# Performance work log

Measured on AMD Instinct MI355X. Metric: run time of the kernel, lower is better.

## Reference

```python
import jax, jax.numpy as jnp
import numpy as np

D = 1024      # n_embd
H = 2048      # expert_hidden_dim
G = 4         # num_groups
EPG = 2       # experts_per_group
NH = 16       # num_heads
HD = D // NH  # head dim
L = 4         # num_layers
V = 32000     # vocab_size
NC = 32000    # num_classes
MAXS = 2048   # max_seq_len
B, S = 2, 1024
TEMP = 1.0    # router_temperature


def setup_inputs() -> dict:
    key = jax.random.key(0)
    ks = jax.random.split(key, 12)
    sc = 0.02
    def n(k, shape):
        return jax.random.normal(k, shape, jnp.float32) * sc
    return {
        "x": jax.random.randint(ks[0], (B, S), 0, V),
        "tok_emb": n(ks[1], (V, D)),
        "pos_emb": n(ks[2], (MAXS, D)),
        "in_proj_w": n(ks[3], (L, 3 * D, D)),
        "in_proj_b": jnp.zeros((L, 3 * D)),
        "out_w": n(ks[4], (L, D, D)),
        "out_b": jnp.zeros((L, D)),
        "ln1_w": jnp.ones((L, D)), "ln1_b": jnp.zeros((L, D)),
        "ln2_w": jnp.ones((L, D)), "ln2_b": jnp.zeros((L, D)),
        "gr_w": n(ks[5], (L, D, G)), "gr_b": jnp.zeros((L, G)),
        "er_w": n(ks[6], (L, G, D, EPG)), "er_b": jnp.zeros((L, G, EPG)),
        "w1": n(ks[7], (L, G, EPG, D, H)), "b1": jnp.zeros((L, G, EPG, H)),
        "w2": n(ks[8], (L, G, EPG, H, D)), "b2": jnp.zeros((L, G, EPG, D)),
        "lnf_w": jnp.ones((D,)), "lnf_b": jnp.zeros((D,)),
        "head_w": n(ks[9], (NC, D)), "head_b": jnp.zeros((NC,)),
    }


def _ln(x, w, b):
    m = x.mean(-1, keepdims=True)
    v = ((x - m) ** 2).mean(-1, keepdims=True)
    return (x - m) * jax.lax.rsqrt(v + 1e-5) * w + b


def _attn(x, wqkv, bqkv, wo, bo, mask):
    b, s, _ = x.shape
    qkv = x @ wqkv.T + bqkv
    q, k, v = jnp.split(qkv, 3, axis=-1)
    def heads(t):
        return t.reshape(b, s, NH, HD).transpose(0, 2, 1, 3)
    q, k, v = heads(q), heads(k), heads(v)
    sc = jnp.einsum('bhqd,bhkd->bhqk', q, k) / np.float32(np.sqrt(HD))
    sc = jnp.where(mask, sc, jnp.float32(-1e30))
    a = jax.nn.softmax(sc, axis=-1)
    o = jnp.einsum('bhqk,bhkd->bhqd', a, v).transpose(0, 2, 1, 3).reshape(b, s, D)
    return o @ wo.T + bo


def _moe(x, gw, gb, ew, eb, w1, b1, w2, b2):
    # x: [T, D] flattened tokens. 2-level routing: top-1 group, top-1 expert in group.
    gp = jax.nn.softmax((x @ gw + gb) / TEMP, axis=-1)                      # [T,G]
    gidx = jnp.argmax(gp, axis=-1)                                          # [T]
    ep = jax.nn.softmax((jnp.einsum('td,gde->tge', x, ew) + eb) / TEMP, -1)  # [T,G,EPG]
    ep_sel = jnp.take_along_axis(ep, gidx[:, None, None], axis=1)[:, 0]     # [T,EPG]
    eidx = jnp.argmax(ep_sel, axis=-1)                                      # [T]
    gate = (jnp.take_along_axis(gp, gidx[:, None], 1)[:, 0]
            * jnp.take_along_axis(ep_sel, eidx[:, None], 1)[:, 0])          # [T]
    hmid = jax.nn.relu(jnp.einsum('td,gedh->tgeh', x, w1) + b1)             # [T,G,EPG,H]
    out = jnp.einsum('tgeh,gehd->tged', hmid, w2) + b2                      # [T,G,EPG,D]
    comb = (jax.nn.one_hot(gidx, G, dtype=x.dtype)[:, :, None]
            * jax.nn.one_hot(eidx, EPG, dtype=x.dtype)[:, None, :]) * gate[:, None, None]
    return jnp.einsum('tge,tged->td', comb, out)


def reference(x, tok_emb, pos_emb, in_proj_w, in_proj_b, out_w, out_b,
              ln1_w, ln1_b, ln2_w, ln2_b, gr_w, gr_b, er_w, er_b,
              w1, b1, w2, b2, lnf_w, lnf_b, head_w, head_b):
    b, s = x.shape
    h = tok_emb[x] + pos_emb[jnp.arange(s)][None]
    mask = jnp.tril(jnp.ones((s, s), bool))
    for l in range(L):
        x1 = _ln(h, ln1_w[l], ln1_b[l])
        h = h + _attn(x1, in_proj_w[l], in_proj_b[l], out_w[l], out_b[l], mask)
        x2 = _ln(h, ln2_w[l], ln2_b[l]).reshape(b * s, D)
        h = h + _moe(x2, gr_w[l], gr_b[l], er_w[l], er_b[l],
                     w1[l], b1[l], w2[l], b2[l]).reshape(b, s, D)
    h = _ln(h, lnf_w, lnf_b).mean(axis=1)
    return h @ head_w.T + head_b
```

## Files before the change

kernel.cpp:

```cpp
#include <hip/hip_runtime.h>
#include <hip/hip_bf16.h>
#include <cstdint>
#include <cstddef>

#define D_   1024
#define H_   2048
#define G_   4
#define EPG_ 2
#define NE_  8
#define NH_  16
#define HD_  64
#define L_   4
#define V_   32000
#define NC_  32000
#define B_   2
#define S_   1024
#define T_   2048
#define MAXBLK_ 24

typedef __attribute__((__ext_vector_type__(8))) __bf16 bf16x8;
typedef __attribute__((__ext_vector_type__(4))) __bf16 bf16x4;
typedef __attribute__((__ext_vector_type__(4))) float  f32x4;

__device__ __forceinline__ void gl_lds16(const void* g, void* l) {
  __builtin_amdgcn_global_load_lds(
      (const __attribute__((address_space(1))) void*)g,
      (__attribute__((address_space(3))) void*)l, 16, 0, 0);
}

__device__ __forceinline__ float wave_sum(float v) {
  #pragma unroll
  for (int o = 32; o >= 1; o >>= 1) v += __shfl_xor(v, o, 64);
  return v;
}

__global__ __launch_bounds__(256) void embed_kernel(const int* __restrict__ x,
    const float* __restrict__ tok, const float* __restrict__ pos,
    float* __restrict__ h) {
  int t = blockIdx.x;
  int tid = threadIdx.x;
  int token = x[t];
  int s = t & (S_ - 1);
  float4 tv = *(const float4*)(tok + (size_t)token * D_ + tid * 4);
  float4 pv = *(const float4*)(pos + (size_t)s * D_ + tid * 4);
  float4 r;
  r.x = tv.x + pv.x; r.y = tv.y + pv.y; r.z = tv.z + pv.z; r.w = tv.w + pv.w;
  *(float4*)(h + (size_t)t * D_ + tid * 4) = r;
}

__device__ __forceinline__ float block_sum256(float v, float* sbuf) {
  v = wave_sum(v);
  int tid = threadIdx.x;
  if ((tid & 63) == 0) sbuf[tid >> 6] = v;
  __syncthreads();
  float r = sbuf[0] + sbuf[1] + sbuf[2] + sbuf[3];
  __syncthreads();
  return r;
}

template<bool F32OUT, bool BFOUT>
__global__ __launch_bounds__(256) void ln_kernel(const float* __restrict__ X,
    const float* __restrict__ w, const float* __restrict__ b,
    float* __restrict__ Yf, __bf16* __restrict__ Yb) {
  __shared__ float sbuf[4];
  int t = blockIdx.x, tid = threadIdx.x;
  const float* xr = X + (size_t)t * D_;
  float4 v = *(const float4*)(xr + tid * 4);
  float sum = v.x + v.y + v.z + v.w;
  float m = block_sum256(sum, sbuf) * (1.0f / D_);
  float dx = v.x - m, dy = v.y - m, dz = v.z - m, dw = v.w - m;
  float vs = dx * dx + dy * dy + dz * dz + dw * dw;
  float var = block_sum256(vs, sbuf) * (1.0f / D_);
  float rs = rsqrtf(var + 1e-5f);
  float4 wv = *(const float4*)(w + tid * 4);
  float4 bv = *(const float4*)(b + tid * 4);
  float4 o;
  o.x = dx * rs * wv.x + bv.x;
  o.y = dy * rs * wv.y + bv.y;
  o.z = dz * rs * wv.z + bv.z;
  o.w = dw * rs * wv.w + bv.w;
  if (F32OUT) *(float4*)(Yf + (size_t)t * D_ + tid * 4) = o;
  if (BFOUT) {
    bf16x4 ob = {(__bf16)o.x, (__bf16)o.y, (__bf16)o.z, (__bf16)o.w};
    *(bf16x4*)(Yb + (size_t)t * D_ + tid * 4) = ob;
  }
}

__global__ __launch_bounds__(256) void ln_route_kernel(const float* __restrict__ X,
    const float* __restrict__ lw, const float* __restrict__ lb,
    const float* __restrict__ gw, const float* __restrict__ gb,
    const float* __restrict__ ew, const float* __restrict__ eb,
    __bf16* __restrict__ Yb, int* __restrict__ eidx, float* __restrict__ gate) {
  int wv = threadIdx.x >> 6, lane = threadIdx.x & 63;
  int t = blockIdx.x * 4 + wv;
  const float* xr = X + (size_t)t * D_;
  float4 xv[4];
  #pragma unroll
  for (int k = 0; k < 4; k++) xv[k] = *(const float4*)(xr + lane * 4 + k * 256);
  float s = 0.f;
  #pragma unroll
  for (int k = 0; k < 4; k++) s += xv[k].x + xv[k].y + xv[k].z + xv[k].w;
  float m = wave_sum(s) * (1.0f / D_);
  float vs = 0.f;
  #pragma unroll
  for (int k = 0; k < 4; k++) {
    float a = xv[k].x - m, b2 = xv[k].y - m, c = xv[k].z - m, d = xv[k].w - m;
    vs += a * a + b2 * b2 + c * c + d * d;
  }
  float rs = rsqrtf(wave_sum(vs) * (1.0f / D_) + 1e-5f);
  float y[4][4];
  #pragma unroll
  for (int k = 0; k < 4; k++) {
    int d0 = lane * 4 + k * 256;
    float4 wv4 = *(const float4*)(lw + d0);
    float4 bv4 = *(const float4*)(lb + d0);
    y[k][0] = (xv[k].x - m) * rs * wv4.x + bv4.x;
    y[k][1] = (xv[k].y - m) * rs * wv4.y + bv4.y;
    y[k][2] = (xv[k].z - m) * rs * wv4.z + bv4.z;
    y[k][3] = (xv[k].w - m) * rs * wv4.w + bv4.w;
    bf16x4 ob = {(__bf16)y[k][0], (__bf16)y[k][1], (__bf16)y[k][2], (__bf16)y[k][3]};
    *(bf16x4*)(Yb + (size_t)t * D_ + d0) = ob;
  }
  float g0 = 0, g1 = 0, g2 = 0, g3 = 0;
  #pragma unroll
  for (int k = 0; k < 4; k++)
    #pragma unroll
    for (int j = 0; j < 4; j++) {
      int d = lane * 4 + k * 256 + j;
      float4 gv = *(const float4*)(gw + (size_t)d * G_);
      float yv = y[k][j];
      g0 += yv * gv.x; g1 += yv * gv.y; g2 += yv * gv.z; g3 += yv * gv.w;
    }
  g0 = wave_sum(g0) + gb[0];
  g1 = wave_sum(g1) + gb[1];
  g2 = wave_sum(g2) + gb[2];
  g3 = wave_sum(g3) + gb[3];
  float mx = fmaxf(fmaxf(g0, g1), fmaxf(g2, g3));
  float p0 = __expf(g0 - mx), p1 = __expf(g1 - mx), p2 = __expf(g2 - mx), p3 = __expf(g3 - mx);
  float psum = p0 + p1 + p2 + p3;
  int gidx = 0; float best = g0;
  if (g1 > best) { best = g1; gidx = 1; }
  if (g2 > best) { best = g2; gidx = 2; }
  if (g3 > best) { best = g3; gidx = 3; }
  float gpsel = ((gidx == 0) ? p0 : (gidx == 1) ? p1 : (gidx == 2) ? p2 : p3) / psum;
  const float* ewg = ew + (size_t)gidx * D_ * EPG_;
  float e0 = 0, e1 = 0;
  #pragma unroll
  for (int k = 0; k < 4; k++)
    #pragma unroll
    for (int j = 0; j < 4; j++) {
      int d = lane * 4 + k * 256 + j;
      float2 ev = *(const float2*)(ewg + (size_t)d * EPG_);
      e0 += y[k][j] * ev.x; e1 += y[k][j] * ev.y;
    }
  e0 = wave_sum(e0) + eb[gidx * EPG_ + 0];
  e1 = wave_sum(e1) + eb[gidx * EPG_ + 1];
  float em = fmaxf(e0, e1);
  float q0 = __expf(e0 - em), q1 = __expf(e1 - em);
  int ei = (e1 > e0) ? 1 : 0;
  float epsel = ((ei == 0) ? q0 : q1) / (q0 + q1);
  if (lane == 0) {
    eidx[t] = gidx * EPG_ + ei;
    gate[t] = gpsel * epsel;
  }
}

__global__ __launch_bounds__(256) void finalize_kernel(const int* __restrict__ eidx,
    int* __restrict__ counts, int* __restrict__ offs, int* __restrict__ tlist,
    int* __restrict__ blk) {
  __shared__ int hist[256][NE_];
  __shared__ int eoff[NE_];
  int tid = threadIdx.x;
  int loc[NE_];
  #pragma unroll
  for (int e = 0; e < NE_; e++) loc[e] = 0;
  int te[8];
  #pragma unroll
  for (int i = 0; i < 8; i++) { te[i] = eidx[tid * 8 + i]; loc[te[i]]++; }
  #pragma unroll
  for (int e = 0; e < NE_; e++) hist[tid][e] = loc[e];
  __syncthreads();
  for (int off = 1; off < 256; off <<= 1) {
    int v[NE_];
    #pragma unroll
    for (int e = 0; e < NE_; e++) v[e] = (tid >= off) ? hist[tid - off][e] : 0;
    __syncthreads();
    #pragma unroll
    for (int e = 0; e < NE_; e++) hist[tid][e] += v[e];
    __syncthreads();
  }
  if (tid == 0) {
    int acc = 0, nb = 0;
    for (int e = 0; e < NE_; e++) {
      int c = hist[255][e];
      eoff[e] = acc; counts[e] = c; offs[e] = acc; acc += c;
      for (int mt = 0; mt * 128 < c; mt++) blk[nb++] = e | (mt << 8);
    }
    for (; nb < MAXBLK_; nb++) blk[nb] = -1;
  }
  __syncthreads();
  int run[NE_];
  #pragma unroll
  for (int e = 0; e < NE_; e++) run[e] = eoff[e] + hist[tid][e] - loc[e];
  #pragma unroll
  for (int i = 0; i < 8; i++) {
    int e = te[i];
    tlist[run[e]++] = tid * 8 + i;
  }
}

template<int MODE, int NF, bool KN>
__global__ __launch_bounds__(256, 2) void gemm_mfma(
    const __bf16* __restrict__ A, const float* __restrict__ W,
    const float* __restrict__ bias, float* __restrict__ Cf,
    __bf16* __restrict__ Cb, const int* __restrict__ tlist,
    const int* __restrict__ offs, const int* __restrict__ counts,
    const float* __restrict__ gate, const int* __restrict__ blk,
    int N, int K) {
  __shared__ __bf16 As[128 * 64];
  __shared__ __bf16 Bs[NF * 32 * 64];
  int e = 0, mt = blockIdx.y, cnt = T_;
  if (MODE >= 2) {
    int bv = blk[blockIdx.y];
    if (bv < 0) return;
    e = bv & 255; mt = bv >> 8;
    cnt = counts[e];
  }
  int row0 = mt * 128;
  int lbase = (MODE >= 2) ? offs[e] : 0;
  int col0 = blockIdx.x * (NF * 32);
  const float* Wp = W + (size_t)e * N * K;
  const float* bp = bias + (size_t)e * N;
  int tid = threadIdx.x;
  int w = tid >> 6, lane = tid & 63, lq = lane & 15, lg = lane >> 4;
  int wr = w >> 1, wc = w & 1;

  const __bf16* asrc[4];
  #pragma unroll
  for (int it = 0; it < 4; it++) {
    int v = it * 256 + tid;
    int r = v >> 3, u = v & 7;
    int gr = row0 + r;
    long rowidx;
    if (MODE >= 2) rowidx = tlist[lbase + ((gr < cnt) ? gr : cnt - 1)];
    else rowidx = gr;
    asrc[it] = A + (size_t)rowidx * K + (u ^ (r & 7)) * 8;
  }
  const float* bsrc[NF];
  int bdst[NF];
  #pragma unroll
  for (int it = 0; it < NF; it++) {
    if (!KN) {
      int v = it * 256 + tid;
      int n = v >> 3, u = v & 7;
      bsrc[it] = Wp + (size_t)(col0 + n) * K + u * 8;
      bdst[it] = n * 64 + (u ^ (n & 7)) * 8;
    } else {
      int v = it * 256 + tid;
      int n = v & (NF * 32 - 1), u = v / (NF * 32);
      bsrc[it] = Wp + (size_t)(u * 8) * N + col0 + n;
      bdst[it] = n * 64 + (u ^ (n & 7)) * 8;
    }
  }

  float br0[NF * 8], br1[NF * 8];
  f32x4 acc[4][NF] = {};

  auto loadB = [&](float* br, int k0) {
    #pragma unroll
    for (int it = 0; it < NF; it++) {
      if (!KN) {
        float4 f0 = *(const float4*)(bsrc[it] + k0);
        float4 f1 = *(const float4*)(bsrc[it] + k0 + 4);
        br[it * 8 + 0] = f0.x; br[it * 8 + 1] = f0.y;
        br[it * 8 + 2] = f0.z; br[it * 8 + 3] = f0.w;
        br[it * 8 + 4] = f1.x; br[it * 8 + 5] = f1.y;
        br[it * 8 + 6] = f1.z; br[it * 8 + 7] = f1.w;
      } else {
        #pragma unroll
        for (int j = 0; j < 8; j++)
          br[it * 8 + j] = bsrc[it][(size_t)(k0 + j) * N];
      }
    }
  };
  auto writeB = [&](const float* br) {
    #pragma unroll
    for (int it = 0; it < NF; it++) {
      bf16x8 bb = {(__bf16)br[it * 8 + 0], (__bf16)br[it * 8 + 1],
                   (__bf16)br[it * 8 + 2], (__bf16)br[it * 8 + 3],
                   (__bf16)br[it * 8 + 4], (__bf16)br[it * 8 + 5],
                   (__bf16)br[it * 8 + 6], (__bf16)br[it * 8 + 7]};
      *(bf16x8*)&Bs[bdst[it]] = bb;
    }
  };
  auto stageA = [&](int k0) {
    #pragma unroll
    for (int it = 0; it < 4; it++)
      gl_lds16(asrc[it] + k0, &As[(it * 256 + tid) * 8]);
  };
  auto mfmaPhase = [&]() {
    #pragma unroll
    for (int kk = 0; kk < 2; kk++) {
      bf16x8 a[4], b[NF];
      int us = ((lg + kk * 4) ^ (lq & 7)) * 8;
      #pragma unroll
      for (int fi = 0; fi < 4; fi++)
        a[fi] = *(const bf16x8*)&As[(wr * 64 + fi * 16 + lq) * 64 + us];
      #pragma unroll
      for (int fj = 0; fj < NF; fj++)
        b[fj] = *(const bf16x8*)&Bs[(wc * (NF * 16) + fj * 16 + lq) * 64 + us];
      #pragma unroll
      for (int fi = 0; fi < 4; fi++)
        #pragma unroll
        for (int fj = 0; fj < NF; fj++)
          acc[fi][fj] = __builtin_amdgcn_mfma_f32_16x16x32_bf16(a[fi], b[fj], acc[fi][fj], 0, 0, 0);
    }
  };

  loadB(br0, 0);
  for (int k0 = 0; k0 < K; k0 += 128) {
    stageA(k0);
    writeB(br0);
    loadB(br1, k0 + 64);
    __syncthreads();
    mfmaPhase();
    __syncthreads();
    stageA(k0 + 64);
    writeB(br1);
    if (k0 + 128 < K) loadB(br0, k0 + 128);
    __syncthreads();
    mfmaPhase();
    __syncthreads();
  }

  #pragma unroll
  for (int fi = 0; fi < 4; fi++) {
    #pragma unroll
    for (int v = 0; v < 4; v++) {
      int r = row0 + wr * 64 + fi * 16 + lg * 4 + v;
      long orow;
      float gv = 1.f;
      if (MODE >= 2) {
        if (r >= cnt) continue;
        orow = tlist[lbase + r];
        if (MODE == 3) gv = gate[orow];
      } else {
        orow = r;
      }
      #pragma unroll
      for (int fj = 0; fj < NF; fj++) {
        int c = col0 + wc * (NF * 16) + fj * 16 + lq;
        float val = acc[fi][fj][v] + bp[c];
        if (MODE == 0)      Cb[orow * N + c] = (__bf16)val;
        else if (MODE == 1) Cf[orow * N + c] += val;
        else if (MODE == 2) Cb[orow * N + c] = (__bf16)fmaxf(val, 0.f);
        else                Cf[orow * N + c] += gv * val;
      }
    }
  }
}

#define SC_LOG2 0.18033688011112042f
__global__ __launch_bounds__(256) void attn_mfma_kernel(const __bf16* __restrict__ qkv,
                                                        __bf16* __restrict__ out) {
  __shared__ __bf16 Ks[64][72];
  __shared__ __bf16 Vt[64][72];
  __shared__ __bf16 Ps[64][72];
  int tid = threadIdx.x;
  int w = tid >> 6, lane = tid & 63, lq = lane & 15, lg = lane >> 4;
  int qt = (S_ / 64 - 1) - blockIdx.x;
  int b = blockIdx.y >> 4, hh = blockIdx.y & 15;
  const __bf16* qbase = qkv + (size_t)b * S_ * 3 * D_ + hh * HD_;

  bf16x8 qa[2];
  {
    const __bf16* qp = qbase + (size_t)(qt * 64 + w * 16 + lq) * 3 * D_ + lg * 8;
    qa[0] = *(const bf16x8*)qp;
    qa[1] = *(const bf16x8*)(qp + 32);
  }

  f32x4 o[4] = {};
  float m_[4] = {-1e30f, -1e30f, -1e30f, -1e30f};
  float l_[4] = {0.f, 0.f, 0.f, 0.f};

  for (int kt = 0; kt <= qt; kt++) {
    #pragma unroll
    for (int it = 0; it < 2; it++) {
      int idx = tid + it * 256;
      int row = idx >> 3, c8 = idx & 7;
      const __bf16* kp = qbase + (size_t)(kt * 64 + row) * 3 * D_ + D_ + c8 * 8;
      *(bf16x8*)&Ks[row][c8 * 8] = *(const bf16x8*)kp;
      bf16x8 vv = *(const bf16x8*)(kp + D_);
      #pragma unroll
      for (int j = 0; j < 8; j++) Vt[c8 * 8 + j][row] = vv[j];
    }
    __syncthreads();

    f32x4 s[4] = {};
    #pragma unroll
    for (int kk = 0; kk < 2; kk++)
      #pragma unroll
      for (int fc = 0; fc < 4; fc++) {
        bf16x8 kf = *(const bf16x8*)&Ks[fc * 16 + lq][lg * 8 + kk * 32];
        s[fc] = __builtin_amdgcn_mfma_f32_16x16x32_bf16(qa[kk], kf, s[fc], 0, 0, 0);
      }

    #pragma unroll
    for (int fc = 0; fc < 4; fc++)
      #pragma unroll
      for (int v = 0; v < 4; v++) {
        float sv = s[fc][v] * SC_LOG2;
        if (kt == qt && (fc * 16 + lq) > (w * 16 + lg * 4 + v)) sv = -1e30f;
        s[fc][v] = sv;
      }

    float corr[4];
    #pragma unroll
    for (int v = 0; v < 4; v++) {
      float rm = fmaxf(fmaxf(s[0][v], s[1][v]), fmaxf(s[2][v], s[3][v]));
      #pragma unroll
      for (int o2 = 8; o2 >= 1; o2 >>= 1) rm = fmaxf(rm, __shfl_xor(rm, o2, 64));
      float mnew = fmaxf(m_[v], rm);
      float cc = exp2f(m_[v] - mnew);
      float rs = 0.f;
      #pragma unroll
      for (int fc = 0; fc < 4; fc++) {
        float p = exp2f(s[fc][v] - mnew);
        s[fc][v] = p; rs += p;
      }
      l_[v] = l_[v] * cc + rs;
      m_[v] = mnew;
      corr[v] = cc;
    }
    #pragma unroll
    for (int dc = 0; dc < 4; dc++)
      #pragma unroll
      for (int v = 0; v < 4; v++) o[dc][v] *= corr[v];

    #pragma unroll
    for (int fc = 0; fc < 4; fc++)
      #pragma unroll
      for (int v = 0; v < 4; v++)
        Ps[w * 16 + lg * 4 + v][fc * 16 + lq] = (__bf16)s[fc][v];
    __syncthreads();

    #pragma unroll
    for (int kk = 0; kk < 2; kk++) {
      bf16x8 pa = *(const bf16x8*)&Ps[w * 16 + lq][lg * 8 + kk * 32];
      #pragma unroll
      for (int dc = 0; dc < 4; dc++) {
        bf16x8 vb = *(const bf16x8*)&Vt[dc * 16 + lq][lg * 8 + kk * 32];
        o[dc] = __builtin_amdgcn_mfma_f32_16x16x32_bf16(pa, vb, o[dc], 0, 0, 0);
      }
    }
    __syncthreads();
  }

  #pragma unroll
  for (int v = 0; v < 4; v++) {
    float ls = l_[v];
    #pragma unroll
    for (int o2 = 8; o2 >= 1; o2 >>= 1) ls += __shfl_xor(ls, o2, 64);
    float inv = 1.0f / ls;
    int row = qt * 64 + w * 16 + lg * 4 + v;
    __bf16* op = out + ((size_t)b * S_ + row) * D_ + hh * HD_;
    #pragma unroll
    for (int dc = 0; dc < 4; dc++)
      op[dc * 16 + lq] = (__bf16)(o[dc][v] * inv);
  }
}

__global__ __launch_bounds__(256) void mean_part_kernel(const float* __restrict__ X,
                                                        float* __restrict__ part) {
  int bd = blockIdx.x * 256 + threadIdx.x;
  int chunk = blockIdx.y;
  int b = bd >> 10, d = bd & 1023;
  float s = 0.f;
  #pragma unroll 4
  for (int i = 0; i < 64; i++) {
    int sidx = chunk * 64 + i;
    s += X[((size_t)b * S_ + sidx) * D_ + d];
  }
  part[chunk * T_ + bd] = s;
}

__global__ __launch_bounds__(256) void mean_final_kernel(const float* __restrict__ part,
                                                         float* __restrict__ hm) {
  int bd = blockIdx.x * 256 + threadIdx.x;
  float s = 0.f;
  #pragma unroll
  for (int c = 0; c < 16; c++) s += part[c * T_ + bd];
  hm[bd] = s * (1.0f / S_);
}

__global__ __launch_bounds__(256) void head_kernel(const float* __restrict__ hm,
    const float* __restrict__ hw, const float* __restrict__ hb,
    float* __restrict__ out) {
  int w = threadIdx.x >> 6;
  int lane = threadIdx.x & 63;
  int c = blockIdx.x * 4 + w;
  const float* row = hw + (size_t)c * D_;
  float acc0 = 0.f, acc1 = 0.f;
  #pragma unroll
  for (int k = 0; k < 4; k++) {
    int d = lane * 4 + k * 256;
    float4 wv = *(const float4*)(row + d);
    float4 h0 = *(const float4*)(hm + d);
    float4 h1 = *(const float4*)(hm + D_ + d);
    acc0 += wv.x * h0.x + wv.y * h0.y + wv.z * h0.z + wv.w * h0.w;
    acc1 += wv.x * h1.x + wv.y * h1.y + wv.z * h1.z + wv.w * h1.w;
  }
  #pragma unroll
  for (int o = 32; o >= 1; o >>= 1) {
    acc0 += __shfl_xor(acc0, o, 64);
    acc1 += __shfl_xor(acc1, o, 64);
  }
  if (lane == 0) {
    float bias = hb[c];
    out[c] = acc0 + bias;
    out[NC_ + c] = acc1 + bias;
  }
}

extern "C" void kernel_launch(void* const* d_in, const int* in_sizes, int n_in,
                              void* d_out, int out_size, void* d_ws, size_t ws_size,
                              hipStream_t stream) {
  const int*   x        = (const int*)d_in[0];
  const float* tok_emb  = (const float*)d_in[1];
  const float* pos_emb  = (const float*)d_in[2];
  const float* in_proj_w= (const float*)d_in[3];
  const float* in_proj_b= (const float*)d_in[4];
  const float* out_w    = (const float*)d_in[5];
  const float* out_b    = (const float*)d_in[6];
  const float* ln1_w    = (const float*)d_in[7];
  const float* ln1_b    = (const float*)d_in[8];
  const float* ln2_w    = (const float*)d_in[9];
  const float* ln2_b    = (const float*)d_in[10];
  const float* gr_w     = (const float*)d_in[11];
  const float* gr_b     = (const float*)d_in[12];
  const float* er_w     = (const float*)d_in[13];
  const float* er_b     = (const float*)d_in[14];
  const float* w1       = (const float*)d_in[15];
  const float* b1       = (const float*)d_in[16];
  const float* w2       = (const float*)d_in[17];
  const float* b2       = (const float*)d_in[18];
  const float* lnf_w    = (const float*)d_in[19];
  const float* lnf_b    = (const float*)d_in[20];
  const float* head_w   = (const float*)d_in[21];
  const float* head_b   = (const float*)d_in[22];

  char* wp = (char*)d_ws;
  auto carve = [&](size_t bytes) -> char* {
    char* p = wp;
    wp += (bytes + 255) & ~(size_t)255;
    return p;
  };
  float*  h      = (float*)carve((size_t)T_ * D_ * 4);
  float*  x1     = (float*)carve((size_t)T_ * D_ * 4);
  __bf16* x1b    = (__bf16*)carve((size_t)T_ * D_ * 2);
  __bf16* qkvb   = (__bf16*)carve((size_t)T_ * 3 * D_ * 2);
  __bf16* attnb  = (__bf16*)carve((size_t)T_ * D_ * 2);
  __bf16* hmidb  = (__bf16*)carve((size_t)T_ * H_ * 2);
  float*  part   = (float*)carve((size_t)16 * T_ * 4);
  float*  hm     = (float*)carve((size_t)B_ * D_ * 4);
  float*  gate   = (float*)carve((size_t)T_ * 4);
  int*    eidx   = (int*)carve((size_t)T_ * 4);
  int*    tlist  = (int*)carve((size_t)T_ * 4);
  int*    counts = (int*)carve(64);
  int*    offs   = (int*)carve(64);
  int*    blk    = (int*)carve(MAXBLK_ * 4);

  embed_kernel<<<T_, 256, 0, stream>>>(x, tok_emb, pos_emb, h);

  for (int l = 0; l < L_; l++) {
    ln_kernel<false, true><<<T_, 256, 0, stream>>>(h, ln1_w + l * D_, ln1_b + l * D_,
                                                   nullptr, x1b);
    gemm_mfma<0, 4, false><<<dim3(24, 16, 1), 256, 0, stream>>>(
        x1b, in_proj_w + (size_t)l * 3 * D_ * D_, in_proj_b + (size_t)l * 3 * D_,
        nullptr, qkvb, nullptr, nullptr, nullptr, nullptr, nullptr, 3 * D_, D_);
    attn_mfma_kernel<<<dim3(S_ / 64, B_ * NH_), 256, 0, stream>>>(qkvb, attnb);
    gemm_mfma<1, 2, false><<<dim3(16, 16, 1), 256, 0, stream>>>(
        attnb, out_w + (size_t)l * D_ * D_, out_b + (size_t)l * D_, h, nullptr,
        nullptr, nullptr, nullptr, nullptr, nullptr, D_, D_);

    ln_route_kernel<<<T_ / 4, 256, 0, stream>>>(h,
        ln2_w + l * D_, ln2_b + l * D_,
        gr_w + (size_t)l * D_ * G_, gr_b + (size_t)l * G_,
        er_w + (size_t)l * G_ * D_ * EPG_, er_b + (size_t)l * G_ * EPG_,
        x1b, eidx, gate);
    finalize_kernel<<<1, 256, 0, stream>>>(eidx, counts, offs, tlist, blk);

    gemm_mfma<2, 4, true><<<dim3(H_ / 128, MAXBLK_, 1), 256, 0, stream>>>(
        x1b, w1 + (size_t)l * NE_ * D_ * H_, b1 + (size_t)l * NE_ * H_, nullptr, hmidb,
        tlist, offs, counts, nullptr, blk, H_, D_);
    gemm_mfma<3, 2, true><<<dim3(D_ / 64, MAXBLK_, 1), 256, 0, stream>>>(
        hmidb, w2 + (size_t)l * NE_ * H_ * D_, b2 + (size_t)l * NE_ * D_, h, nullptr,
        tlist, offs, counts, gate, blk, D_, H_);
  }

  ln_kernel<true, false><<<T_, 256, 0, stream>>>(h, lnf_w, lnf_b, x1, nullptr);
  mean_part_kernel<<<dim3(B_ * D_ / 256, 16), 256, 0, stream>>>(x1, part);
  mean_final_kernel<<<B_ * D_ / 256, 256, 0, stream>>>(part, hm);
  head_kernel<<<NC_ / 4, 256, 0, stream>>>(hm, head_w, head_b, (float*)d_out);
}
```

Before: 906.0 us.

## Widen attention query tile to 128 rows, swizzle V transpose, compact MoE hidden rows

The attention kernel now runs 512 threads per block over a 128-row query tile, so each K/V tile staged in shared memory serves twice as many query rows and fewer blocks are launched. Each wave skips key tiles that lie entirely above its causal diagonal, applies the mask only on tiles that cross the diagonal, and rescales the running max only when it increases. The transposed V buffer is XOR-swizzled to cut shared-memory bank conflicts, and one block-wide barrier per key tile is dropped in favour of a compiler memory fence. Separately, the MoE first GEMM now writes hidden rows in compact expert-sorted order, so the second GEMM reads them contiguously instead of through the token list. The trade-offs are fewer, larger attention blocks and more causal imbalance between waves, plus reliance on wave-private Ps rows being safe without a barrier.

```diff
diff --git a/kernel.cpp b/kernel.cpp
--- a/kernel.cpp
+++ b/kernel.cpp
@@ -17,6 +17,7 @@
 #define S_   1024
 #define T_   2048
 #define MAXBLK_ 24
+#define QB_  128
 
 typedef __attribute__((__ext_vector_type__(8))) __bf16 bf16x8;
 typedef __attribute__((__ext_vector_type__(4))) __bf16 bf16x4;
@@ -242,7 +243,8 @@
     int r = v >> 3, u = v & 7;
     int gr = row0 + r;
     long rowidx;
-    if (MODE >= 2) rowidx = tlist[lbase + ((gr < cnt) ? gr : cnt - 1)];
+    if (MODE == 2) rowidx = tlist[lbase + ((gr < cnt) ? gr : cnt - 1)];
+    else if (MODE == 3) rowidx = lbase + ((gr < cnt) ? gr : cnt - 1);
     else rowidx = gr;
     asrc[it] = A + (size_t)rowidx * K + (u ^ (r & 7)) * 8;
   }
@@ -342,8 +344,8 @@
       float gv = 1.f;
       if (MODE >= 2) {
         if (r >= cnt) continue;
-        orow = tlist[lbase + r];
-        if (MODE == 3) gv = gate[orow];
+        if (MODE == 2) orow = lbase + r;
+        else { orow = tlist[lbase + r]; gv = gate[orow]; }
       } else {
         orow = r;
       }
@@ -361,20 +363,20 @@
 }
 
 #define SC_LOG2 0.18033688011112042f
-__global__ __launch_bounds__(256) void attn_mfma_kernel(const __bf16* __restrict__ qkv,
+__global__ __launch_bounds__(512) void attn_mfma_kernel(const __bf16* __restrict__ qkv,
                                                         __bf16* __restrict__ out) {
   __shared__ __bf16 Ks[64][72];
   __shared__ __bf16 Vt[64][72];
-  __shared__ __bf16 Ps[64][72];
+  __shared__ __bf16 Ps[QB_][72];
   int tid = threadIdx.x;
   int w = tid >> 6, lane = tid & 63, lq = lane & 15, lg = lane >> 4;
-  int qt = (S_ / 64 - 1) - blockIdx.x;
+  int qt = (S_ / QB_ - 1) - blockIdx.x;
   int b = blockIdx.y >> 4, hh = blockIdx.y & 15;
   const __bf16* qbase = qkv + (size_t)b * S_ * 3 * D_ + hh * HD_;
 
   bf16x8 qa[2];
   {
-    const __bf16* qp = qbase + (size_t)(qt * 64 + w * 16 + lq) * 3 * D_ + lg * 8;
+    const __bf16* qp = qbase + (size_t)(qt * QB_ + w * 16 + lq) * 3 * D_ + lg * 8;
     qa[0] = *(const bf16x8*)qp;
     qa[1] = *(const bf16x8*)(qp + 32);
   }
@@ -383,74 +385,75 @@
   float m_[4] = {-1e30f, -1e30f, -1e30f, -1e30f};
   float l_[4] = {0.f, 0.f, 0.f, 0.f};
 
-  for (int kt = 0; kt <= qt; kt++) {
-    #pragma unroll
-    for (int it = 0; it < 2; it++) {
-      int idx = tid + it * 256;
-      int row = idx >> 3, c8 = idx & 7;
-      const __bf16* kp = qbase + (size_t)(kt * 64 + row) * 3 * D_ + D_ + c8 * 8;
-      *(bf16x8*)&Ks[row][c8 * 8] = *(const bf16x8*)kp;
+  int rowmin = qt * QB_ + w * 16;
+  int srow = tid >> 3, sc8 = tid & 7;
+  int nkt = qt * 2 + 2;
+
+  for (int kt = 0; kt < nkt; kt++) {
+    {
+      const __bf16* kp = qbase + (size_t)(kt * 64 + srow) * 3 * D_ + D_ + sc8 * 8;
+      *(bf16x8*)&Ks[srow][sc8 * 8] = *(const bf16x8*)kp;
       bf16x8 vv = *(const bf16x8*)(kp + D_);
-      #pragma unroll
-      for (int j = 0; j < 8; j++) Vt[c8 * 8 + j][row] = vv[j];
-    }
-    __syncthreads();
-
-    f32x4 s[4] = {};
-    #pragma unroll
-    for (int kk = 0; kk < 2; kk++)
-      #pragma unroll
-      for (int fc = 0; fc < 4; fc++) {
-        bf16x8 kf = *(const bf16x8*)&Ks[fc * 16 + lq][lg * 8 + kk * 32];
-        s[fc] = __builtin_amdgcn_mfma_f32_16x16x32_bf16(qa[kk], kf, s[fc], 0, 0, 0);
+      int cs = srow ^ (sc8 << 3);
+      #pragma unroll
+      for (int j = 0; j < 8; j++) Vt[sc8 * 8 + j][cs] = vv[j];
+    }
+    __syncthreads();
+
+    if (kt * 64 <= rowmin + 15) {
+      f32x4 s[4] = {};
+      #pragma unroll
+      for (int kk = 0; kk < 2; kk++)
+        #pragma unroll
+        for (int fc = 0; fc < 4; fc++) {
+          bf16x8 kf = *(const bf16x8*)&Ks[fc * 16 + lq][lg * 8 + kk * 32];
+          s[fc] = __builtin_amdgcn_mfma_f32_16x16x32_bf16(qa[kk], kf, s[fc], 0, 0, 0);
+        }
+
+      bool need_mask = (kt * 64 + 63 > rowmin);
+      #pragma unroll
+      for (int fc = 0; fc < 4; fc++)
+        #pragma unroll
+        for (int v = 0; v < 4; v++) {
+          float sv = s[fc][v] * SC_LOG2;
+          if (need_mask && (kt * 64 + fc * 16 + lq) > (rowmin + lg * 4 + v)) sv = -1e30f;
+          s[fc][v] = sv;
+        }
+
+      #pragma unroll
+      for (int v = 0; v < 4; v++) {
+        float rm = fmaxf(fmaxf(s[0][v], s[1][v]), fmaxf(s[2][v], s[3][v]));
+        #pragma unroll
+        for (int o2 = 8; o2 >= 1; o2 >>= 1) rm = fmaxf(rm, __shfl_xor(rm, o2, 64));
+        if (rm > m_[v]) {
+          float cc = exp2f(m_[v] - rm);
+          m_[v] = rm;
+          l_[v] *= cc;
+          o[0][v] *= cc; o[1][v] *= cc; o[2][v] *= cc; o[3][v] *= cc;
+        }
+        float rs = 0.f;
+        #pragma unroll
+        for (int fc = 0; fc < 4; fc++) {
+          float p = exp2f(s[fc][v] - m_[v]);
+          s[fc][v] = p; rs += p;
+        }
+        l_[v] += rs;
+        #pragma unroll
+        for (int fc = 0; fc < 4; fc++)
+          Ps[w * 16 + lg * 4 + v][fc * 16 + lq] = (__bf16)s[fc][v];
       }
-
-    #pragma unroll
-    for (int fc = 0; fc < 4; fc++)
-      #pragma unroll
-      for (int v = 0; v < 4; v++) {
-        float sv = s[fc][v] * SC_LOG2;
-        if (kt == qt && (fc * 16 + lq) > (w * 16 + lg * 4 + v)) sv = -1e30f;
-        s[fc][v] = sv;
-      }
-
-    float corr[4];
-    #pragma unroll
-    for (int v = 0; v < 4; v++) {
-      float rm = fmaxf(fmaxf(s[0][v], s[1][v]), fmaxf(s[2][v], s[3][v]));
-      #pragma unroll
-      for (int o2 = 8; o2 >= 1; o2 >>= 1) rm = fmaxf(rm, __shfl_xor(rm, o2, 64));
-      float mnew = fmaxf(m_[v], rm);
-      float cc = exp2f(m_[v] - mnew);
-      float rs = 0.f;
-      #pragma unroll
-      for (int fc = 0; fc < 4; fc++) {
-        float p = exp2f(s[fc][v] - mnew);
-        s[fc][v] = p; rs += p;
-      }
-      l_[v] = l_[v] * cc + rs;
-      m_[v] = mnew;
-      corr[v] = cc;
-    }
-    #pragma unroll
-    for (int dc = 0; dc < 4; dc++)
-      #pragma unroll
-      for (int v = 0; v < 4; v++) o[dc][v] *= corr[v];
-
-    #pragma unroll
-    for (int fc = 0; fc < 4; fc++)
-      #pragma unroll
-      for (int v = 0; v < 4; v++)
-        Ps[w * 16 + lg * 4 + v][fc * 16 + lq] = (__bf16)s[fc][v];
-    __syncthreads();
-
-    #pragma unroll
-    for (int kk = 0; kk < 2; kk++) {
-      bf16x8 pa = *(const bf16x8*)&Ps[w * 16 + lq][lg * 8 + kk * 32];
-      #pragma unroll
-      for (int dc = 0; dc < 4; dc++) {
-        bf16x8 vb = *(const bf16x8*)&Vt[dc * 16 + lq][lg * 8 + kk * 32];
-        o[dc] = __builtin_amdgcn_mfma_f32_16x16x32_bf16(pa, vb, o[dc], 0, 0, 0);
+      asm volatile("" ::: "memory");
+
+      #pragma unroll
+      for (int kk = 0; kk < 2; kk++) {
+        bf16x8 pa = *(const bf16x8*)&Ps[w * 16 + lq][lg * 8 + kk * 32];
+        #pragma unroll
+        for (int dc = 0; dc < 4; dc++) {
+          int d = dc * 16 + lq;
+          int col = (lg * 8 + kk * 32) ^ ((d >> 3) << 3);
+          bf16x8 vb = *(const bf16x8*)&Vt[d][col];
+          o[dc] = __builtin_amdgcn_mfma_f32_16x16x32_bf16(pa, vb, o[dc], 0, 0, 0);
+        }
       }
     }
     __syncthreads();
@@ -462,7 +465,7 @@
     #pragma unroll
     for (int o2 = 8; o2 >= 1; o2 >>= 1) ls += __shfl_xor(ls, o2, 64);
     float inv = 1.0f / ls;
-    int row = qt * 64 + w * 16 + lg * 4 + v;
+    int row = rowmin + lg * 4 + v;
     __bf16* op = out + ((size_t)b * S_ + row) * D_ + hh * HD_;
     #pragma unroll
     for (int dc = 0; dc < 4; dc++)
@@ -578,7 +581,7 @@
     gemm_mfma<0, 4, false><<<dim3(24, 16, 1), 256, 0, stream>>>(
         x1b, in_proj_w + (size_t)l * 3 * D_ * D_, in_proj_b + (size_t)l * 3 * D_,
         nullptr, qkvb, nullptr, nullptr, nullptr, nullptr, nullptr, 3 * D_, D_);
-    attn_mfma_kernel<<<dim3(S_ / 64, B_ * NH_), 256, 0, stream>>>(qkvb, attnb);
+    attn_mfma_kernel<<<dim3(S_ / QB_, B_ * NH_), 512, 0, stream>>>(qkvb, attnb);
     gemm_mfma<1, 2, false><<<dim3(16, 16, 1), 256, 0, stream>>>(
         attnb, out_w + (size_t)l * D_ * D_, out_b + (size_t)l * D_, h, nullptr,
         nullptr, nullptr, nullptr, nullptr, nullptr, D_, D_);
```

Result: faster. 888.2 us (-2.0%).
